# Performance work log

Hardware: AMD Instinct MI355X
Metric: run time of the kernel (lower is better)

Reference implementation:

```python
import jax, jax.numpy as jnp
import numpy as np

B_SZ, L, H, P = 8, 8192, 1024, 64  # batch, seq, d_inner, ssm_size
CONJ_SYM = True
DT_MIN, DT_MAX, DT_FLOOR = 1e-3, 1e-1, 1e-4


def setup_inputs() -> dict:
    key = jax.random.key(0)
    ks = jax.random.split(key, 8)
    u = jax.random.normal(ks[0], (B_SZ, L, H), dtype=jnp.float32)
    h_real = jnp.zeros((B_SZ, P), dtype=jnp.float32)
    h_imag = jnp.zeros((B_SZ, P), dtype=jnp.float32)
    # HiPPO-like stable init: Re(Lambda) = -0.5, Im(Lambda) = pi*k
    A_real = -0.5 * jnp.ones((P,), dtype=jnp.float32)
    A_imag = jnp.pi * jnp.arange(P, dtype=jnp.float32)
    local_P = 2 * P if CONJ_SYM else P
    b_scale = np.sqrt(1.0 / local_P).astype(np.float32)
    c_scale = np.sqrt(1.0 / H).astype(np.float32)
    B_real = jax.random.normal(ks[1], (P, H), dtype=jnp.float32) * b_scale
    B_imag = jax.random.normal(ks[2], (P, H), dtype=jnp.float32) * b_scale
    C_real = jax.random.normal(ks[3], (H, P), dtype=jnp.float32) * c_scale
    C_imag = jax.random.normal(ks[4], (H, P), dtype=jnp.float32) * c_scale
    D = jax.random.normal(ks[5], (H,), dtype=jnp.float32)
    # torch init: dt = exp(U(log dt_min, log dt_max)).clamp(dt_floor); inv_dt = dt + log(-expm1(-dt))
    log_dt = jax.random.uniform(ks[6], (P,), dtype=jnp.float32) \
        * (np.log(DT_MAX) - np.log(DT_MIN)) + np.log(DT_MIN)
    dt0 = jnp.clip(jnp.exp(log_dt), DT_FLOOR, None)
    inv_dt = dt0 + jnp.log(-jnp.expm1(-dt0))
    return {"u": u, "h_real": h_real, "h_imag": h_imag,
            "A_real": A_real, "A_imag": A_imag,
            "B_real": B_real, "B_imag": B_imag,
            "C_real": C_real, "C_imag": C_imag,
            "D": D, "inv_dt": inv_dt}


def reference(u, h_real, h_imag, A_real, A_imag, B_real, B_imag,
              C_real, C_imag, D, inv_dt):
    A = A_real + 1j * A_imag            # (P,)
    Bm = B_real + 1j * B_imag           # (P, H)
    Cm = C_real + 1j * C_imag           # (H, P)
    dt = jax.nn.softplus(inv_dt)        # step_rescale = 1.0
    # bilinear discretization
    den = 1.0 - (dt / 2.0) * A
    dA = (1.0 + (dt / 2.0) * A) / den   # (P,)
    dB = (dt / den)[:, None] * Bm       # (P, H)
    # input projection: Bu[b,l,p] = sum_h dB[p,h] * u[b,l,h]
    Bu = jnp.einsum('blh,ph->blp', u, dB)              # complex64 (B, L, P)
    h0 = h_real + 1j * h_imag                          # (B, P)
    Bu = Bu.at[:, 0].add(dA * h0)                      # fold initial state in
    a = jnp.broadcast_to(dA, Bu.shape)
    def combine(e1, e2):
        a1, b1 = e1
        a2, b2 = e2
        return a2 * a1, a2 * b1 + b2
    _, hs = jax.lax.associative_scan(combine, (a, Bu), axis=1)  # (B, L, P)
    yc = jnp.einsum('blp,hp->blh', hs, Cm)
    scale = 2.0 if CONJ_SYM else 1.0
    y = scale * yc.real + D * u
    h_last = hs[:, -1]
    return y, h_last.real, h_last.imag
```

## Files before the change

### kernel.cpp

```cpp
#include <hip/hip_runtime.h>

typedef unsigned short ushort_t;
typedef short s8v __attribute__((ext_vector_type(8)));
typedef unsigned short ushort8 __attribute__((ext_vector_type(8)));
typedef float floatx4 __attribute__((ext_vector_type(4)));

#define MFMA16(a, b, c) __builtin_amdgcn_mfma_f32_16x16x32_bf16((a), (b), (c), 0, 0, 0)

static constexpr int B_SZ = 8;
static constexpr int L = 8192;
static constexpr int H = 1024;
static constexpr int P = 64;
static constexpr int M_TOT = B_SZ * L;
static constexpr int S_CH = 256;
static constexpr int NC = L / S_CH;

__device__ inline ushort_t f2bf(float f) {
    union { float f; unsigned u; } v; v.f = f;
    unsigned r = v.u + 0x7fffu + ((v.u >> 16) & 1u);
    return (ushort_t)(r >> 16);
}

__global__ void params_kernel(const float* __restrict__ A_real,
                              const float* __restrict__ A_imag,
                              const float* __restrict__ inv_dt,
                              float* __restrict__ params,
                              float* __restrict__ dApow) {
    int p = threadIdx.x;
    float x = inv_dt[p];
    float dt = (x > 20.f) ? x : log1pf(expf(x));
    float ar = A_real[p], ai = A_imag[p];
    float dr = 1.f - 0.5f * dt * ar;
    float di = -0.5f * dt * ai;
    float inv = 1.f / fmaf(dr, dr, di * di);
    float nr = 1.f + 0.5f * dt * ar, ni = 0.5f * dt * ai;
    float dAr = (nr * dr + ni * di) * inv;
    float dAi = (ni * dr - nr * di) * inv;
    params[p]       = dAr;
    params[64 + p]  = dAi;
    params[128 + p] = dt * dr * inv;
    params[192 + p] = -dt * di * inv;
    float pr = 1.f, pi = 0.f;
    dApow[p] = 1.f; dApow[64 + p] = 0.f;
    for (int k = 1; k <= S_CH; k++) {
        float npr = pr * dAr - pi * dAi;
        float npi = pr * dAi + pi * dAr;
        pr = npr; pi = npi;
        dApow[k * 128 + p] = pr;
        dApow[k * 128 + 64 + p] = pi;
    }
}

__global__ void build_w(const float* __restrict__ Br, const float* __restrict__ Bi,
                        const float* __restrict__ Cr, const float* __restrict__ Ci,
                        const float* __restrict__ params,
                        ushort_t* __restrict__ W1T, ushort_t* __restrict__ CeffT) {
    int t = blockIdx.x * 256 + threadIdx.x;
    if (t < 128 * 1024) {
        int n = t >> 10, k = t & 1023;
        float v;
        if (n < 64) {
            float sr = params[128 + n], si = params[192 + n];
            v = sr * Br[n * 1024 + k] - si * Bi[n * 1024 + k];
        } else {
            int p = n - 64;
            float sr = params[128 + p], si = params[192 + p];
            v = sr * Bi[p * 1024 + k] + si * Br[p * 1024 + k];
        }
        W1T[t] = f2bf(v);
    } else {
        int t2 = t - 128 * 1024;
        int h = t2 >> 7, k = t2 & 127;
        float v = (k < 64) ? 2.f * Cr[h * 64 + k] : -2.f * Ci[h * 64 + (k - 64)];
        CeffT[t2] = f2bf(v);
    }
}

__global__ __launch_bounds__(256) void gemm1(const float* __restrict__ u,
                                             const ushort_t* __restrict__ W1T,
                                             float* __restrict__ Bu) {
    __shared__ ushort_t As[128][40];
    __shared__ ushort_t Bs[128][40];
    int tid = threadIdx.x;
    int wave = tid >> 6, lane = tid & 63;
    int q = lane >> 4, mn = lane & 15;
    size_t row0 = (size_t)blockIdx.x * 128;
    int r = tid >> 1, half = tid & 1;

    floatx4 acc[2][8] = {};

    for (int kk = 0; kk < 1024; kk += 32) {
        __syncthreads();
        {
            const float4* up = (const float4*)(u + (row0 + r) * 1024 + kk + half * 16);
            float4 f0 = up[0], f1 = up[1], f2 = up[2], f3 = up[3];
            ushort8 t0, t1;
            t0[0] = f2bf(f0.x); t0[1] = f2bf(f0.y); t0[2] = f2bf(f0.z); t0[3] = f2bf(f0.w);
            t0[4] = f2bf(f1.x); t0[5] = f2bf(f1.y); t0[6] = f2bf(f1.z); t0[7] = f2bf(f1.w);
            t1[0] = f2bf(f2.x); t1[1] = f2bf(f2.y); t1[2] = f2bf(f2.z); t1[3] = f2bf(f2.w);
            t1[4] = f2bf(f3.x); t1[5] = f2bf(f3.y); t1[6] = f2bf(f3.z); t1[7] = f2bf(f3.w);
            ushort8* dst = (ushort8*)&As[r][half * 16];
            dst[0] = t0; dst[1] = t1;
            const ushort8* wp = (const ushort8*)(W1T + r * 1024 + kk + half * 16);
            ushort8* db = (ushort8*)&Bs[r][half * 16];
            db[0] = wp[0]; db[1] = wp[1];
        }
        __syncthreads();
        s8v a0 = *(const s8v*)&As[wave * 32 + mn][q * 8];
        s8v a1 = *(const s8v*)&As[wave * 32 + 16 + mn][q * 8];
        #pragma unroll
        for (int j = 0; j < 8; j++) {
            s8v bf = *(const s8v*)&Bs[j * 16 + mn][q * 8];
            acc[0][j] = MFMA16(a0, bf, acc[0][j]);
            acc[1][j] = MFMA16(a1, bf, acc[1][j]);
        }
    }
    #pragma unroll
    for (int i = 0; i < 2; i++)
        #pragma unroll
        for (int j = 0; j < 8; j++)
            #pragma unroll
            for (int reg = 0; reg < 4; reg++) {
                size_t row = row0 + wave * 32 + i * 16 + q * 4 + reg;
                Bu[row * 128 + j * 16 + mn] = acc[i][j][reg];
            }
}

__global__ void scan_local(float* __restrict__ Bu, const float* __restrict__ params,
                           const float* __restrict__ h0r, const float* __restrict__ h0i,
                           float* __restrict__ endbuf) {
    int b = blockIdx.x >> 5;
    int c = blockIdx.x & 31;
    int p = threadIdx.x;
    float dAr = params[p], dAi = params[64 + p];
    size_t base = ((size_t)b * L + (size_t)c * S_CH) * 128 + p;
    float hr = 0.f, hi = 0.f;
    for (int l = 0; l < S_CH; l++) {
        float br = Bu[base + (size_t)l * 128];
        float bi = Bu[base + (size_t)l * 128 + 64];
        if (c == 0 && l == 0) {
            float r0 = h0r[b * 64 + p], i0 = h0i[b * 64 + p];
            br += dAr * r0 - dAi * i0;
            bi += dAr * i0 + dAi * r0;
        }
        float nhr = fmaf(dAr, hr, fmaf(-dAi, hi, br));
        float nhi = fmaf(dAr, hi, fmaf(dAi, hr, bi));
        hr = nhr; hi = nhi;
        Bu[base + (size_t)l * 128] = hr;
        Bu[base + (size_t)l * 128 + 64] = hi;
    }
    endbuf[((size_t)b * NC + c) * 128 + p] = hr;
    endbuf[((size_t)b * NC + c) * 128 + 64 + p] = hi;
}

__global__ void scan_carry(const float* __restrict__ endbuf,
                           const float* __restrict__ dApow,
                           float* __restrict__ carry) {
    int t = blockIdx.x * 64 + threadIdx.x;
    int b = t >> 6, p = t & 63;
    float aSr = dApow[S_CH * 128 + p], aSi = dApow[S_CH * 128 + 64 + p];
    float cr = 0.f, ci = 0.f;
    for (int c = 0; c < NC; c++) {
        carry[((size_t)b * NC + c) * 128 + p] = cr;
        carry[((size_t)b * NC + c) * 128 + 64 + p] = ci;
        float er = endbuf[((size_t)b * NC + c) * 128 + p];
        float ei = endbuf[((size_t)b * NC + c) * 128 + 64 + p];
        float nr = fmaf(aSr, cr, fmaf(-aSi, ci, er));
        float ni = fmaf(aSr, ci, fmaf(aSi, cr, ei));
        cr = nr; ci = ni;
    }
}

__global__ __launch_bounds__(256) void fixup(const float* __restrict__ hloc,
                                             const float* __restrict__ carry,
                                             const float* __restrict__ dApow,
                                             ushort_t* __restrict__ hfix,
                                             float* __restrict__ out_hlast) {
    size_t t = (size_t)blockIdx.x * 256 + threadIdx.x;
    size_t r = t >> 6; int p = (int)(t & 63);
    int b = (int)(r >> 13);
    int l = (int)(r & 8191);
    int c = l >> 8;
    int k = (l & (S_CH - 1)) + 1;
    float pr = dApow[k * 128 + p], pi = dApow[k * 128 + 64 + p];
    float cr = carry[((size_t)b * NC + c) * 128 + p];
    float ci = carry[((size_t)b * NC + c) * 128 + 64 + p];
    float hr = hloc[r * 128 + p] + pr * cr - pi * ci;
    float hi = hloc[r * 128 + 64 + p] + pr * ci + pi * cr;
    hfix[r * 128 + p] = f2bf(hr);
    hfix[r * 128 + 64 + p] = f2bf(hi);
    if (l == L - 1) {
        out_hlast[b * 64 + p] = hr;
        out_hlast[512 + b * 64 + p] = hi;
    }
}

__global__ __launch_bounds__(256) void gemm2(const ushort_t* __restrict__ hfix,
                                             const ushort_t* __restrict__ CeffT,
                                             const float* __restrict__ u,
                                             const float* __restrict__ D,
                                             float* __restrict__ y) {
    __shared__ ushort_t As[128][136];
    __shared__ ushort_t Bs[128][136];
    int tid = threadIdx.x;
    int wave = tid >> 6, lane = tid & 63;
    int q = lane >> 4, mn = lane & 15;
    size_t row0 = (size_t)blockIdx.x * 128;
    int r = tid >> 1, half = tid & 1;
    {
        const ushort8* src = (const ushort8*)(hfix + (row0 + r) * 128 + half * 64);
        ushort8* dst = (ushort8*)&As[r][half * 64];
        #pragma unroll
        for (int i = 0; i < 8; i++) dst[i] = src[i];
    }
    for (int ct = 0; ct < 8; ct++) {
        __syncthreads();
        {
            const ushort8* src = (const ushort8*)(CeffT + (size_t)(ct * 128 + r) * 128 + half * 64);
            ushort8* dst = (ushort8*)&Bs[r][half * 64];
            #pragma unroll
            for (int i = 0; i < 8; i++) dst[i] = src[i];
        }
        __syncthreads();
        floatx4 acc[2][8] = {};
        #pragma unroll
        for (int kk = 0; kk < 128; kk += 32) {
            s8v a0 = *(const s8v*)&As[wave * 32 + mn][kk + q * 8];
            s8v a1 = *(const s8v*)&As[wave * 32 + 16 + mn][kk + q * 8];
            #pragma unroll
            for (int j = 0; j < 8; j++) {
                s8v bf = *(const s8v*)&Bs[j * 16 + mn][kk + q * 8];
                acc[0][j] = MFMA16(a0, bf, acc[0][j]);
                acc[1][j] = MFMA16(a1, bf, acc[1][j]);
            }
        }
        float dv[8];
        #pragma unroll
        for (int j = 0; j < 8; j++) dv[j] = D[ct * 128 + j * 16 + mn];
        #pragma unroll
        for (int i = 0; i < 2; i++)
            #pragma unroll
            for (int j = 0; j < 8; j++) {
                int col = ct * 128 + j * 16 + mn;
                #pragma unroll
                for (int reg = 0; reg < 4; reg++) {
                    size_t row = row0 + wave * 32 + i * 16 + q * 4 + reg;
                    y[row * 1024 + col] = acc[i][j][reg] + dv[j] * u[row * 1024 + col];
                }
            }
    }
}

extern "C" void kernel_launch(void* const* d_in, const int* in_sizes, int n_in,
                              void* d_out, int out_size, void* d_ws, size_t ws_size,
                              hipStream_t stream) {
    const float* u      = (const float*)d_in[0];
    const float* h_r    = (const float*)d_in[1];
    const float* h_i    = (const float*)d_in[2];
    const float* A_real = (const float*)d_in[3];
    const float* A_imag = (const float*)d_in[4];
    const float* B_real = (const float*)d_in[5];
    const float* B_imag = (const float*)d_in[6];
    const float* C_real = (const float*)d_in[7];
    const float* C_imag = (const float*)d_in[8];
    const float* D      = (const float*)d_in[9];
    const float* inv_dt = (const float*)d_in[10];
    float* out = (float*)d_out;

    float* wsf       = (float*)d_ws;
    float* P_params  = wsf;
    float* P_dApow   = wsf + 1024;
    float* P_carry   = wsf + 1024 + 33024;
    float* P_end     = P_carry + 32768;
    ushort_t* P_W1T  = (ushort_t*)(P_end + 32768);
    ushort_t* P_Ceff = P_W1T + 128 * 1024;
    float* P_Bu      = (float*)(P_Ceff + 1024 * 128);
    ushort_t* P_hfix = (ushort_t*)(P_Bu + (size_t)M_TOT * 128);

    params_kernel<<<1, 64, 0, stream>>>(A_real, A_imag, inv_dt, P_params, P_dApow);
    build_w<<<1024, 256, 0, stream>>>(B_real, B_imag, C_real, C_imag, P_params, P_W1T, P_Ceff);
    gemm1<<<M_TOT / 128, 256, 0, stream>>>(u, P_W1T, P_Bu);
    scan_local<<<B_SZ * NC, 64, 0, stream>>>(P_Bu, P_params, h_r, h_i, P_end);
    scan_carry<<<8, 64, 0, stream>>>(P_end, P_dApow, P_carry);
    fixup<<<(M_TOT * 64) / 256, 256, 0, stream>>>(P_Bu, P_carry, P_dApow, P_hfix,
                                                  out + (size_t)M_TOT * H);
    gemm2<<<M_TOT / 128, 256, 0, stream>>>(P_hfix, P_Ceff, u, D, out);
}
```

Before: 622.2 us.

## Fuse scan fixup into gemm2, interleave complex layout, shrink scan chunks

Removes the separate fixup kernel and its bf16 hfix buffer. gemm2 now reads the local scan states, applies the carry times the dA powers while staging its A tile, and writes h_last itself. The state layout changes from split real/imag halves to interleaved real/imag pairs, so the scan can use float2 loads and stores. Chunk size drops from 256 to 64, which gives four times as many chunks and raises scan_local parallelism, at the cost of a longer serial carry scan and extra fp32 reads in gemm2's prologue.

```diff
diff --git a/kernel.cpp b/kernel.cpp
--- a/kernel.cpp
+++ b/kernel.cpp
@@ -12,7 +12,7 @@
 static constexpr int H = 1024;
 static constexpr int P = 64;
 static constexpr int M_TOT = B_SZ * L;
-static constexpr int S_CH = 256;
+static constexpr int S_CH = 64;
 static constexpr int NC = L / S_CH;
 
 __device__ inline ushort_t f2bf(float f) {
@@ -41,13 +41,13 @@
     params[128 + p] = dt * dr * inv;
     params[192 + p] = -dt * di * inv;
     float pr = 1.f, pi = 0.f;
-    dApow[p] = 1.f; dApow[64 + p] = 0.f;
+    dApow[2 * p] = 1.f; dApow[2 * p + 1] = 0.f;
     for (int k = 1; k <= S_CH; k++) {
         float npr = pr * dAr - pi * dAi;
         float npi = pr * dAi + pi * dAr;
         pr = npr; pi = npi;
-        dApow[k * 128 + p] = pr;
-        dApow[k * 128 + 64 + p] = pi;
+        dApow[k * 128 + 2 * p]     = pr;
+        dApow[k * 128 + 2 * p + 1] = pi;
     }
 }
 
@@ -58,20 +58,16 @@
     int t = blockIdx.x * 256 + threadIdx.x;
     if (t < 128 * 1024) {
         int n = t >> 10, k = t & 1023;
-        float v;
-        if (n < 64) {
-            float sr = params[128 + n], si = params[192 + n];
-            v = sr * Br[n * 1024 + k] - si * Bi[n * 1024 + k];
-        } else {
-            int p = n - 64;
-            float sr = params[128 + p], si = params[192 + p];
-            v = sr * Bi[p * 1024 + k] + si * Br[p * 1024 + k];
-        }
+        int p = n >> 1;
+        float sr = params[128 + p], si = params[192 + p];
+        float br = Br[p * 1024 + k], bi = Bi[p * 1024 + k];
+        float v = (n & 1) ? (sr * bi + si * br) : (sr * br - si * bi);
         W1T[t] = f2bf(v);
     } else {
         int t2 = t - 128 * 1024;
         int h = t2 >> 7, k = t2 & 127;
-        float v = (k < 64) ? 2.f * Cr[h * 64 + k] : -2.f * Ci[h * 64 + (k - 64)];
+        int p = k >> 1;
+        float v = (k & 1) ? -2.f * Ci[h * 64 + p] : 2.f * Cr[h * 64 + p];
         CeffT[t2] = f2bf(v);
     }
 }
@@ -126,80 +122,59 @@
             }
 }
 
-__global__ void scan_local(float* __restrict__ Bu, const float* __restrict__ params,
-                           const float* __restrict__ h0r, const float* __restrict__ h0i,
-                           float* __restrict__ endbuf) {
-    int b = blockIdx.x >> 5;
-    int c = blockIdx.x & 31;
-    int p = threadIdx.x;
+__global__ __launch_bounds__(256) void scan_local(float* __restrict__ Bu,
+                                                  const float* __restrict__ params,
+                                                  float* __restrict__ endbuf) {
+    int tid = threadIdx.x;
+    int p = tid & 63;
+    int chunk = blockIdx.x * 4 + (tid >> 6);
+    int b = chunk >> 7, c = chunk & (NC - 1);
     float dAr = params[p], dAi = params[64 + p];
-    size_t base = ((size_t)b * L + (size_t)c * S_CH) * 128 + p;
+    float* base = Bu + ((size_t)b * L + (size_t)c * S_CH) * 128 + 2 * p;
     float hr = 0.f, hi = 0.f;
+    float2 cur = *(const float2*)base;
+    float2 nxt;
+    #pragma unroll 4
     for (int l = 0; l < S_CH; l++) {
-        float br = Bu[base + (size_t)l * 128];
-        float bi = Bu[base + (size_t)l * 128 + 64];
-        if (c == 0 && l == 0) {
-            float r0 = h0r[b * 64 + p], i0 = h0i[b * 64 + p];
-            br += dAr * r0 - dAi * i0;
-            bi += dAr * i0 + dAi * r0;
-        }
-        float nhr = fmaf(dAr, hr, fmaf(-dAi, hi, br));
-        float nhi = fmaf(dAr, hi, fmaf(dAi, hr, bi));
+        if (l < S_CH - 1) nxt = *(const float2*)(base + (size_t)(l + 1) * 128);
+        float nhr = fmaf(dAr, hr, fmaf(-dAi, hi, cur.x));
+        float nhi = fmaf(dAr, hi, fmaf(dAi, hr, cur.y));
         hr = nhr; hi = nhi;
-        Bu[base + (size_t)l * 128] = hr;
-        Bu[base + (size_t)l * 128 + 64] = hi;
-    }
-    endbuf[((size_t)b * NC + c) * 128 + p] = hr;
-    endbuf[((size_t)b * NC + c) * 128 + 64 + p] = hi;
+        *(float2*)(base + (size_t)l * 128) = make_float2(hr, hi);
+        cur = nxt;
+    }
+    float* e = endbuf + (size_t)chunk * 128 + 2 * p;
+    e[0] = hr; e[1] = hi;
 }
 
 __global__ void scan_carry(const float* __restrict__ endbuf,
                            const float* __restrict__ dApow,
+                           const float* __restrict__ h0r,
+                           const float* __restrict__ h0i,
                            float* __restrict__ carry) {
     int t = blockIdx.x * 64 + threadIdx.x;
     int b = t >> 6, p = t & 63;
-    float aSr = dApow[S_CH * 128 + p], aSi = dApow[S_CH * 128 + 64 + p];
-    float cr = 0.f, ci = 0.f;
+    float aSr = dApow[S_CH * 128 + 2 * p], aSi = dApow[S_CH * 128 + 2 * p + 1];
+    float cr = h0r[b * 64 + p], ci = h0i[b * 64 + p];
     for (int c = 0; c < NC; c++) {
-        carry[((size_t)b * NC + c) * 128 + p] = cr;
-        carry[((size_t)b * NC + c) * 128 + 64 + p] = ci;
-        float er = endbuf[((size_t)b * NC + c) * 128 + p];
-        float ei = endbuf[((size_t)b * NC + c) * 128 + 64 + p];
+        float* dst = carry + ((size_t)b * NC + c) * 128 + 2 * p;
+        dst[0] = cr; dst[1] = ci;
+        const float* e = endbuf + ((size_t)b * NC + c) * 128 + 2 * p;
+        float er = e[0], ei = e[1];
         float nr = fmaf(aSr, cr, fmaf(-aSi, ci, er));
         float ni = fmaf(aSr, ci, fmaf(aSi, cr, ei));
         cr = nr; ci = ni;
     }
 }
 
-__global__ __launch_bounds__(256) void fixup(const float* __restrict__ hloc,
-                                             const float* __restrict__ carry,
-                                             const float* __restrict__ dApow,
-                                             ushort_t* __restrict__ hfix,
-                                             float* __restrict__ out_hlast) {
-    size_t t = (size_t)blockIdx.x * 256 + threadIdx.x;
-    size_t r = t >> 6; int p = (int)(t & 63);
-    int b = (int)(r >> 13);
-    int l = (int)(r & 8191);
-    int c = l >> 8;
-    int k = (l & (S_CH - 1)) + 1;
-    float pr = dApow[k * 128 + p], pi = dApow[k * 128 + 64 + p];
-    float cr = carry[((size_t)b * NC + c) * 128 + p];
-    float ci = carry[((size_t)b * NC + c) * 128 + 64 + p];
-    float hr = hloc[r * 128 + p] + pr * cr - pi * ci;
-    float hi = hloc[r * 128 + 64 + p] + pr * ci + pi * cr;
-    hfix[r * 128 + p] = f2bf(hr);
-    hfix[r * 128 + 64 + p] = f2bf(hi);
-    if (l == L - 1) {
-        out_hlast[b * 64 + p] = hr;
-        out_hlast[512 + b * 64 + p] = hi;
-    }
-}
-
-__global__ __launch_bounds__(256) void gemm2(const ushort_t* __restrict__ hfix,
+__global__ __launch_bounds__(256) void gemm2(const float* __restrict__ hloc,
                                              const ushort_t* __restrict__ CeffT,
                                              const float* __restrict__ u,
                                              const float* __restrict__ D,
-                                             float* __restrict__ y) {
+                                             const float* __restrict__ dApow,
+                                             const float* __restrict__ carry,
+                                             float* __restrict__ y,
+                                             float* __restrict__ out_hlast) {
     __shared__ ushort_t As[128][136];
     __shared__ ushort_t Bs[128][136];
     int tid = threadIdx.x;
@@ -208,10 +183,41 @@
     size_t row0 = (size_t)blockIdx.x * 128;
     int r = tid >> 1, half = tid & 1;
     {
-        const ushort8* src = (const ushort8*)(hfix + (row0 + r) * 128 + half * 64);
+        size_t rrow = row0 + r;
+        int b = (int)(rrow >> 13);
+        int l = (int)(rrow & (L - 1));
+        int c = l >> 6;
+        int kp = (l & (S_CH - 1)) + 1;
+        const float4* hp = (const float4*)(hloc + rrow * 128 + half * 64);
+        const float4* pw = (const float4*)(dApow + (size_t)kp * 128 + half * 64);
+        const float4* cv = (const float4*)(carry + ((size_t)b * NC + c) * 128 + half * 64);
         ushort8* dst = (ushort8*)&As[r][half * 64];
-        #pragma unroll
-        for (int i = 0; i < 8; i++) dst[i] = src[i];
+        bool last = (l == L - 1);
+        #pragma unroll
+        for (int j = 0; j < 8; j++) {
+            float4 hv0 = hp[2 * j], hv1 = hp[2 * j + 1];
+            float4 p0 = pw[2 * j], p1 = pw[2 * j + 1];
+            float4 c0 = cv[2 * j], c1 = cv[2 * j + 1];
+            float r0 = hv0.x + p0.x * c0.x - p0.y * c0.y;
+            float i0 = hv0.y + p0.x * c0.y + p0.y * c0.x;
+            float r1 = hv0.z + p0.z * c0.z - p0.w * c0.w;
+            float i1 = hv0.w + p0.z * c0.w + p0.w * c0.z;
+            float r2 = hv1.x + p1.x * c1.x - p1.y * c1.y;
+            float i2 = hv1.y + p1.x * c1.y + p1.y * c1.x;
+            float r3 = hv1.z + p1.z * c1.z - p1.w * c1.w;
+            float i3 = hv1.w + p1.z * c1.w + p1.w * c1.z;
+            ushort8 o;
+            o[0] = f2bf(r0); o[1] = f2bf(i0); o[2] = f2bf(r1); o[3] = f2bf(i1);
+            o[4] = f2bf(r2); o[5] = f2bf(i2); o[6] = f2bf(r3); o[7] = f2bf(i3);
+            dst[j] = o;
+            if (last) {
+                int pb = (half * 64 + j * 8) >> 1;
+                out_hlast[b * 64 + pb]           = r0; out_hlast[512 + b * 64 + pb]     = i0;
+                out_hlast[b * 64 + pb + 1]       = r1; out_hlast[512 + b * 64 + pb + 1] = i1;
+                out_hlast[b * 64 + pb + 2]       = r2; out_hlast[512 + b * 64 + pb + 2] = i2;
+                out_hlast[b * 64 + pb + 3]       = r3; out_hlast[512 + b * 64 + pb + 3] = i3;
+            }
+        }
     }
     for (int ct = 0; ct < 8; ct++) {
         __syncthreads();
@@ -270,19 +276,17 @@
     float* wsf       = (float*)d_ws;
     float* P_params  = wsf;
     float* P_dApow   = wsf + 1024;
-    float* P_carry   = wsf + 1024 + 33024;
-    float* P_end     = P_carry + 32768;
-    ushort_t* P_W1T  = (ushort_t*)(P_end + 32768);
+    float* P_carry   = wsf + 1024 + 8448;
+    float* P_end     = P_carry + 131072;
+    ushort_t* P_W1T  = (ushort_t*)(P_end + 131072);
     ushort_t* P_Ceff = P_W1T + 128 * 1024;
     float* P_Bu      = (float*)(P_Ceff + 1024 * 128);
-    ushort_t* P_hfix = (ushort_t*)(P_Bu + (size_t)M_TOT * 128);
 
     params_kernel<<<1, 64, 0, stream>>>(A_real, A_imag, inv_dt, P_params, P_dApow);
     build_w<<<1024, 256, 0, stream>>>(B_real, B_imag, C_real, C_imag, P_params, P_W1T, P_Ceff);
     gemm1<<<M_TOT / 128, 256, 0, stream>>>(u, P_W1T, P_Bu);
-    scan_local<<<B_SZ * NC, 64, 0, stream>>>(P_Bu, P_params, h_r, h_i, P_end);
-    scan_carry<<<8, 64, 0, stream>>>(P_end, P_dApow, P_carry);
-    fixup<<<(M_TOT * 64) / 256, 256, 0, stream>>>(P_Bu, P_carry, P_dApow, P_hfix,
-                                                  out + (size_t)M_TOT * H);
-    gemm2<<<M_TOT / 128, 256, 0, stream>>>(P_hfix, P_Ceff, u, D, out);
-}
+    scan_local<<<B_SZ * NC / 4, 256, 0, stream>>>(P_Bu, P_params, P_end);
+    scan_carry<<<8, 64, 0, stream>>>(P_end, P_dApow, h_r, h_i, P_carry);
+    gemm2<<<M_TOT / 128, 256, 0, stream>>>(P_Bu, P_Ceff, u, D, P_dApow, P_carry,
+                                           out, out + (size_t)M_TOT * H);
+}
```

Measured after the change: 605.8 us. 1.03x faster.
